# Performance work log

Hardware: AMD Instinct MI355X
Metric: run time of the kernel (lower is better)

## Reference

```python
import jax, jax.numpy as jnp
import numpy as np

B, S, H = 2, 2048, 4096
NQ, NKV, D = 32, 8, 128
THETA = 10000.0


def setup_inputs() -> dict:
    key = jax.random.key(0)
    k0, k1, k2 = jax.random.split(key, 3)
    hidden_states = jax.random.normal(k0, (B, S, H), dtype=jnp.float32)
    w_qkv = jax.random.normal(k1, (H, (NQ + 2 * NKV) * D), dtype=jnp.float32) * 0.02
    w_o = jax.random.normal(k2, (NQ * D, H), dtype=jnp.float32) * 0.02
    positions = jnp.broadcast_to(jnp.arange(S, dtype=jnp.int32)[None, :], (B, S))
    return {"hidden_states": hidden_states, "w_qkv": w_qkv, "w_o": w_o,
            "positions": positions}


def _rope_gptj(x, cos, sin):
    # non-neox (GPT-J interleaved) RoPE; x: [B,S,h,D], cos/sin: [B,S,1,D/2]
    x1 = x[..., 0::2]
    x2 = x[..., 1::2]
    o1 = x1 * cos - x2 * sin
    o2 = x2 * cos + x1 * sin
    return jnp.stack([o1, o2], axis=-1).reshape(x.shape)


def reference(hidden_states, w_qkv, w_o, positions):
    scale = D ** -0.5
    qkv = hidden_states @ w_qkv  # [B,S,(NQ+2NKV)*D]
    q, k, v = jnp.split(qkv, [NQ * D, (NQ + NKV) * D], axis=-1)
    q = q.reshape(B, S, NQ, D)
    k = k.reshape(B, S, NKV, D)
    v = v.reshape(B, S, NKV, D)

    inv_freq = 1.0 / (THETA ** (jnp.arange(0, D, 2, dtype=jnp.float32) / D))
    freqs = positions.astype(jnp.float32)[..., None] * inv_freq  # [B,S,D/2]
    cos = jnp.cos(freqs)[:, :, None, :]
    sin = jnp.sin(freqs)[:, :, None, :]
    q = _rope_gptj(q, cos, sin)
    k = _rope_gptj(k, cos, sin)

    # GQA: expand kv heads to query heads
    rep = NQ // NKV
    k = jnp.repeat(k, rep, axis=2)  # [B,S,NQ,D]
    v = jnp.repeat(v, rep, axis=2)

    scores = jnp.einsum('bqhd,bkhd->bhqk', q, k) * scale
    causal = jnp.tril(jnp.ones((S, S), dtype=bool))
    scores = jnp.where(causal[None, None, :, :], scores, jnp.finfo(scores.dtype).min)
    probs = jax.nn.softmax(scores, axis=-1)
    attn = jnp.einsum('bhqk,bkhd->bqhd', probs, v).reshape(B, S, NQ * D)
    return attn @ w_o  # [B,S,H]
```

## Files before the change

kernel.cpp:

```cpp
#include <hip/hip_runtime.h>
#include <hip/hip_bf16.h>
#include <stdint.h>

#define B_  2
#define S_  2048
#define H_  4096
#define NQ_ 32
#define NKV_ 8
#define D_  128
#define NQKV_ 6144

typedef __bf16 bf16_t;
typedef __bf16 bf16x4 __attribute__((ext_vector_type(4)));
typedef __bf16 bf16x8 __attribute__((ext_vector_type(8)));
typedef float  floatx4 __attribute__((ext_vector_type(4)));

#define GLOBAL_AS __attribute__((address_space(1)))
#define LDS_AS    __attribute__((address_space(3)))

#define QSCALE (0.08838834764831845f * 1.4426950408889634f)

__global__ __launch_bounds__(256) void convert_f32_bf16(
    const float* __restrict__ src, bf16_t* __restrict__ dst, int n4) {
  int i = blockIdx.x * 256 + threadIdx.x;
  if (i < n4) {
    float4 v = ((const float4*)src)[i];
    bf16_t o[4] = {(bf16_t)v.x, (bf16_t)v.y, (bf16_t)v.z, (bf16_t)v.w};
    ((uint64_t*)dst)[i] = *(const uint64_t*)o;
  }
}

__global__ __launch_bounds__(256) void transpose_f32_bf16(
    const float* __restrict__ src, bf16_t* __restrict__ dst, int R, int C) {
  __shared__ bf16_t tile[64][65];
  const int ct = blockIdx.x * 64, rt = blockIdx.y * 64;
  const int t = threadIdx.x;
  const int cl = t & 63;
  for (int i = 0; i < 16; ++i) {
    int rl = i * 4 + (t >> 6);
    tile[rl][cl] = (bf16_t)src[(size_t)(rt + rl) * C + ct + cl];
  }
  __syncthreads();
  const int rl2 = t & 63;
  for (int i = 0; i < 16; ++i) {
    int cl2 = i * 4 + (t >> 6);
    dst[(size_t)(ct + cl2) * R + rt + rl2] = tile[rl2][cl2];
  }
}

template <typename OutT>
__global__ __launch_bounds__(256) void gemm_abt(
    const bf16_t* __restrict__ A, const bf16_t* __restrict__ Bt,
    OutT* __restrict__ C, int M, int N, int K) {
  __shared__ __align__(16) bf16_t lA[128 * 32];
  __shared__ __align__(16) bf16_t lB[128 * 32];
  const int tid = threadIdx.x;
  const int wave = tid >> 6, lane = tid & 63;
  const int lrow = lane & 15, quad = lane >> 4;
  const int row0 = blockIdx.y * 128, col0 = blockIdx.x * 128;
  const int wm = (wave >> 1) * 64, wn = (wave & 1) * 64;
  const int rA = lane >> 2;
  const int kA = (lane & 3) * 8;

  floatx4 acc[4][4] = {};

  for (int kt = 0; kt < K; kt += 32) {
    __syncthreads();
    for (int j = 0; j < 2; ++j) {
      const int c = wave * 2 + j;
      const bf16_t* ga = A  + (size_t)(row0 + c * 16 + rA) * K + kt + kA;
      const bf16_t* gb = Bt + (size_t)(col0 + c * 16 + rA) * K + kt + kA;
      __builtin_amdgcn_global_load_lds((GLOBAL_AS void*)ga,
                                       (LDS_AS void*)(lA + c * 512), 16, 0, 0);
      __builtin_amdgcn_global_load_lds((GLOBAL_AS void*)gb,
                                       (LDS_AS void*)(lB + c * 512), 16, 0, 0);
    }
    __syncthreads();
    bf16x8 af[4], bfr[4];
    for (int i = 0; i < 4; ++i)
      af[i] = *(const bf16x8*)(lA + (wm + i * 16 + lrow) * 32 + quad * 8);
    for (int j = 0; j < 4; ++j)
      bfr[j] = *(const bf16x8*)(lB + (wn + j * 16 + lrow) * 32 + quad * 8);
    for (int i = 0; i < 4; ++i)
      for (int j = 0; j < 4; ++j)
        acc[i][j] = __builtin_amdgcn_mfma_f32_16x16x32_bf16(af[i], bfr[j],
                                                            acc[i][j], 0, 0, 0);
  }

  for (int i = 0; i < 4; ++i)
    for (int j = 0; j < 4; ++j)
      for (int r = 0; r < 4; ++r) {
        int row = row0 + wm + i * 16 + quad * 4 + r;
        int col = col0 + wn + j * 16 + lrow;
        C[(size_t)row * N + col] = (OutT)acc[i][j][r];
      }
}

__global__ __launch_bounds__(256) void rope_qk(
    const bf16_t* __restrict__ qkv, const int* __restrict__ positions,
    bf16_t* __restrict__ Q, bf16_t* __restrict__ K) {
  const int row = blockIdx.x;
  const int b = row >> 11, s = row & (S_ - 1);
  const float pos = (float)positions[row];
  const bf16_t* src = qkv + (size_t)row * NQKV_;
  for (int p = threadIdx.x; p < (NQ_ + NKV_) * 64; p += 256) {
    const int head = p >> 6, i = p & 63;
    const float inv = __powf(10000.0f, -(float)i * (1.0f / 64.0f));
    const float f = pos * inv;
    const float cs = __cosf(f), sn = __sinf(f);
    const float x1 = (float)src[head * 128 + 2 * i];
    const float x2 = (float)src[head * 128 + 2 * i + 1];
    float o1 = x1 * cs - x2 * sn;
    float o2 = x2 * cs + x1 * sn;
    bf16_t* dst;
    if (head < NQ_) {
      o1 *= QSCALE;
      o2 *= QSCALE;
      dst = Q + ((size_t)(b * NQ_ + head) * S_ + s) * D_ + 2 * i;
    } else {
      dst = K + ((size_t)(b * NKV_ + (head - NQ_)) * S_ + s) * D_ + 2 * i;
    }
    dst[0] = (bf16_t)o1;
    dst[1] = (bf16_t)o2;
  }
}

__global__ __launch_bounds__(256) void v_transpose(
    const bf16_t* __restrict__ qkv, bf16_t* __restrict__ Vt) {
  __shared__ bf16_t tile[64][65];
  const int b = blockIdx.z;
  const int kh = blockIdx.y >> 1;
  const int dt = (blockIdx.y & 1) * 64;
  const int st = blockIdx.x * 64;
  const int t = threadIdx.x;
  const int colbase = (NQ_ + NKV_) * D_ + kh * D_ + dt;
  for (int i = 0; i < 16; ++i) {
    int sl = i * 4 + (t >> 6);
    int dl = t & 63;
    tile[sl][dl] = qkv[(size_t)(b * S_ + st + sl) * NQKV_ + colbase + dl];
  }
  __syncthreads();
  for (int i = 0; i < 16; ++i) {
    int dl = i * 4 + (t >> 6);
    int sl = t & 63;
    Vt[((size_t)(b * NKV_ + kh) * D_ + dt + dl) * S_ + st + sl] = tile[sl][dl];
  }
}

__global__ __launch_bounds__(256) void flash_attn(
    const bf16_t* __restrict__ Q, const bf16_t* __restrict__ K,
    const bf16_t* __restrict__ Vt, bf16_t* __restrict__ O) {
  const int qt = (S_ / 64 - 1) - blockIdx.x;
  const int h  = blockIdx.y;
  const int b  = blockIdx.z;
  const int kh = h >> 2;
  const int tid = threadIdx.x, wave = tid >> 6, lane = tid & 63;
  const int lrow = lane & 15, quad = lane >> 4;
  const int q0 = qt * 64;

  __shared__ __align__(16) char lKb[64 * 256];
  __shared__ __align__(16) char lVb[128 * 128];
  __shared__ __align__(16) char lPb[64 * 128];

#define LK(r, c) (lKb + ((r) << 8) + ((c) ^ (((r) & 7) << 4)))
#define LV(r, c) (lVb + ((r) << 7) + ((c) ^ (((r) & 7) << 4)))
#define LP(r, c) (lPb + ((r) << 7) + ((c) ^ (((r) & 7) << 4)))

  const bf16_t* Qbase = Q  + ((size_t)(b * NQ_ + h) * S_) * D_;
  const bf16_t* Kbase = K  + ((size_t)(b * NKV_ + kh) * S_) * D_;
  const bf16_t* Vbase = Vt + ((size_t)(b * NKV_ + kh) * D_) * S_;

  const int qrow = q0 + wave * 16 + lrow;
  bf16x8 qf[4];
  {
    const bf16_t* qp = Qbase + (size_t)qrow * D_ + quad * 8;
    for (int ks = 0; ks < 4; ++ks) qf[ks] = *(const bf16x8*)(qp + ks * 32);
  }

  const int krow = tid >> 4;
  const int kcol = ((((tid & 15) << 4)) ^ ((krow & 7) << 4)) >> 1;
  const int vrow = tid >> 3;
  const int vcol = ((((tid & 7) << 4)) ^ ((vrow & 7) << 4)) >> 1;

  floatx4 acc[8] = {};
  float mrun = -3.0e38f, lrun = 0.0f;

  const int nkt = qt + 1;
  for (int kt = 0; kt < nkt; ++kt) {
    const int k0 = kt * 64;
    __syncthreads();
#pragma unroll
    for (int i = 0; i < 4; ++i) {
      const bf16_t* ga = Kbase + (size_t)(k0 + i * 16 + krow) * D_ + kcol;
      __builtin_amdgcn_global_load_lds((GLOBAL_AS void*)ga,
          (LDS_AS void*)(lKb + i * 4096 + wave * 1024), 16, 0, 0);
    }
#pragma unroll
    for (int i = 0; i < 4; ++i) {
      const bf16_t* ga = Vbase + (size_t)(i * 32 + vrow) * S_ + k0 + vcol;
      __builtin_amdgcn_global_load_lds((GLOBAL_AS void*)ga,
          (LDS_AS void*)(lVb + i * 4096 + wave * 1024), 16, 0, 0);
    }
    __syncthreads();

    floatx4 sacc[4];
#pragma unroll
    for (int t = 0; t < 4; ++t) {
      floatx4 a = {0.f, 0.f, 0.f, 0.f};
#pragma unroll
      for (int ks = 0; ks < 4; ++ks) {
        bf16x8 kf = *(const bf16x8*)LK(t * 16 + lrow, ks * 64 + quad * 16);
        a = __builtin_amdgcn_mfma_f32_16x16x32_bf16(kf, qf[ks], a, 0, 0, 0);
      }
      sacc[t] = a;
    }

    if (kt == qt) {
#pragma unroll
      for (int t = 0; t < 4; ++t)
#pragma unroll
        for (int r = 0; r < 4; ++r) {
          const int kpos = k0 + t * 16 + quad * 4 + r;
          if (kpos > qrow) sacc[t][r] = -3.0e38f;
        }
    }

    float mx = -3.0e38f;
#pragma unroll
    for (int t = 0; t < 4; ++t)
#pragma unroll
      for (int r = 0; r < 4; ++r) mx = fmaxf(mx, sacc[t][r]);
    mx = fmaxf(mx, __shfl_xor(mx, 16));
    mx = fmaxf(mx, __shfl_xor(mx, 32));

    float mcur = mrun;
    if (!__all(mx - mrun <= 8.0f)) {
      const float mnew = fmaxf(mrun, mx);
      const float alpha = exp2f(mrun - mnew);
      lrun *= alpha;
#pragma unroll
      for (int dt = 0; dt < 8; ++dt) acc[dt] *= alpha;
      mrun = mnew;
      mcur = mnew;
    }

    float rs = 0.0f;
#pragma unroll
    for (int t = 0; t < 4; ++t) {
      bf16x4 pk;
#pragma unroll
      for (int r = 0; r < 4; ++r) {
        float p = exp2f(sacc[t][r] - mcur);
        rs += p;
        pk[r] = (bf16_t)p;
      }
      *(bf16x4*)LP(wave * 16 + lrow, t * 32 + quad * 8) = pk;
    }
    rs += __shfl_xor(rs, 16);
    rs += __shfl_xor(rs, 32);
    lrun += rs;

    bf16x8 pf0 = *(const bf16x8*)LP(wave * 16 + lrow, quad * 16);
    bf16x8 pf1 = *(const bf16x8*)LP(wave * 16 + lrow, 64 + quad * 16);
#pragma unroll
    for (int dt = 0; dt < 8; ++dt) {
      bf16x8 v0 = *(const bf16x8*)LV(dt * 16 + lrow, quad * 16);
      bf16x8 v1 = *(const bf16x8*)LV(dt * 16 + lrow, 64 + quad * 16);
      floatx4 a = acc[dt];
      a = __builtin_amdgcn_mfma_f32_16x16x32_bf16(v0, pf0, a, 0, 0, 0);
      a = __builtin_amdgcn_mfma_f32_16x16x32_bf16(v1, pf1, a, 0, 0, 0);
      acc[dt] = a;
    }
  }

  const float inv_l = 1.0f / lrun;
  bf16_t* Obase = O + ((size_t)(b * S_) + qrow) * (NQ_ * D_) + h * D_;
#pragma unroll
  for (int dt = 0; dt < 8; ++dt) {
    bf16x4 ov;
#pragma unroll
    for (int r = 0; r < 4; ++r) ov[r] = (bf16_t)(acc[dt][r] * inv_l);
    *(bf16x4*)(Obase + dt * 16 + quad * 4) = ov;
  }
#undef LK
#undef LV
#undef LP
}

extern "C" void kernel_launch(void* const* d_in, const int* in_sizes, int n_in,
                              void* d_out, int out_size, void* d_ws, size_t ws_size,
                              hipStream_t stream) {
  const float* hs    = (const float*)d_in[0];
  const float* w_qkv = (const float*)d_in[1];
  const float* w_o   = (const float*)d_in[2];
  const int*   pos   = (const int*)d_in[3];
  float* out = (float*)d_out;

  char* ws = (char*)d_ws;
  constexpr size_t OFF_WT  = 0;
  constexpr size_t OFF_QKV = 50331648;
  constexpr size_t OFF_Q   = OFF_QKV + 50331648;
  constexpr size_t OFF_K   = OFF_Q + 33554432;
  constexpr size_t OFF_VT  = OFF_K + 8388608;
  bf16_t* wT    = (bf16_t*)(ws + OFF_WT);
  bf16_t* qkv   = (bf16_t*)(ws + OFF_QKV);
  bf16_t* Qb    = (bf16_t*)(ws + OFF_Q);
  bf16_t* Kb    = (bf16_t*)(ws + OFF_K);
  bf16_t* Vtb   = (bf16_t*)(ws + OFF_VT);
  bf16_t* hsb   = Qb;
  bf16_t* attnO = qkv;

  convert_f32_bf16<<<dim3((B_ * S_ * H_ / 4) / 256), 256, 0, stream>>>(
      hs, hsb, B_ * S_ * H_ / 4);
  transpose_f32_bf16<<<dim3(NQKV_ / 64, H_ / 64), 256, 0, stream>>>(
      w_qkv, wT, H_, NQKV_);
  gemm_abt<bf16_t><<<dim3(NQKV_ / 128, (B_ * S_) / 128), 256, 0, stream>>>(
      hsb, wT, qkv, B_ * S_, NQKV_, H_);
  rope_qk<<<dim3(B_ * S_), 256, 0, stream>>>(qkv, pos, Qb, Kb);
  v_transpose<<<dim3(S_ / 64, NKV_ * 2, B_), 256, 0, stream>>>(qkv, Vtb);
  transpose_f32_bf16<<<dim3(H_ / 64, (NQ_ * D_) / 64), 256, 0, stream>>>(
      w_o, wT, NQ_ * D_, H_);
  flash_attn<<<dim3(S_ / 64, NQ_, B_), 256, 0, stream>>>(Qb, Kb, Vtb, attnO);
  gemm_abt<float><<<dim3(H_ / 128, (B_ * S_) / 128), 256, 0, stream>>>(
      attnO, wT, out, B_ * S_, H_, H_);

  (void)in_sizes; (void)n_in; (void)out_size; (void)ws_size;
}
```

Before: 901.0 us.

## Rewrite GEMM with 256x256 tiles, double-buffered LDS, swizzle and XCD remap

Replaces the 128x128, single-buffered, K=32 GEMM with a 256x256-tile, 512-thread kernel. It uses K=64 steps, double-buffered async global-to-LDS loads with partial vmcnt waits, an XOR-swizzled LDS layout to avoid bank conflicts, and a block-id remap across 8 chiplets. The goal is more data reuse per tile and overlap of loads with MFMA work in both projection GEMMs. In exchange it uses 128KB of LDS per block and more accumulator registers, and the grid shrinks to 384 and 256 blocks, which may leave some compute units idle.

```diff
diff --git a/kernel.cpp b/kernel.cpp
--- a/kernel.cpp
+++ b/kernel.cpp
@@ -49,50 +49,108 @@
 }
 
 template <typename OutT>
-__global__ __launch_bounds__(256) void gemm_abt(
+__global__ __launch_bounds__(512, 2) void gemm_abt256(
     const bf16_t* __restrict__ A, const bf16_t* __restrict__ Bt,
     OutT* __restrict__ C, int M, int N, int K) {
-  __shared__ __align__(16) bf16_t lA[128 * 32];
-  __shared__ __align__(16) bf16_t lB[128 * 32];
+  __shared__ __align__(16) char lds[131072];
+
+  const int nbx = gridDim.x;
+  const int nwg = nbx * gridDim.y;
+  int bid = blockIdx.y * nbx + blockIdx.x;
+  bid = (bid & 7) * (nwg >> 3) + (bid >> 3);
+  const int bx = bid % nbx, by = bid / nbx;
+
   const int tid = threadIdx.x;
   const int wave = tid >> 6, lane = tid & 63;
   const int lrow = lane & 15, quad = lane >> 4;
-  const int row0 = blockIdx.y * 128, col0 = blockIdx.x * 128;
-  const int wm = (wave >> 1) * 64, wn = (wave & 1) * 64;
-  const int rA = lane >> 2;
-  const int kA = (lane & 3) * 8;
-
-  floatx4 acc[4][4] = {};
-
-  for (int kt = 0; kt < K; kt += 32) {
-    __syncthreads();
-    for (int j = 0; j < 2; ++j) {
-      const int c = wave * 2 + j;
-      const bf16_t* ga = A  + (size_t)(row0 + c * 16 + rA) * K + kt + kA;
-      const bf16_t* gb = Bt + (size_t)(col0 + c * 16 + rA) * K + kt + kA;
-      __builtin_amdgcn_global_load_lds((GLOBAL_AS void*)ga,
-                                       (LDS_AS void*)(lA + c * 512), 16, 0, 0);
-      __builtin_amdgcn_global_load_lds((GLOBAL_AS void*)gb,
-                                       (LDS_AS void*)(lB + c * 512), 16, 0, 0);
-    }
-    __syncthreads();
-    bf16x8 af[4], bfr[4];
-    for (int i = 0; i < 4; ++i)
-      af[i] = *(const bf16x8*)(lA + (wm + i * 16 + lrow) * 32 + quad * 8);
-    for (int j = 0; j < 4; ++j)
-      bfr[j] = *(const bf16x8*)(lB + (wn + j * 16 + lrow) * 32 + quad * 8);
-    for (int i = 0; i < 4; ++i)
-      for (int j = 0; j < 4; ++j)
-        acc[i][j] = __builtin_amdgcn_mfma_f32_16x16x32_bf16(af[i], bfr[j],
-                                                            acc[i][j], 0, 0, 0);
-  }
-
-  for (int i = 0; i < 4; ++i)
-    for (int j = 0; j < 4; ++j)
+  const int wm = (wave >> 2) * 128;
+  const int wn = (wave & 3) * 64;
+  const int row0 = by * 256, col0 = bx * 256;
+
+  const int lr = lane >> 3;
+  const int lc = ((((lane & 7) << 4) ^ (lr << 4)) >> 1);
+
+  auto stage = [&](int buf, int kt) {
+    char* aB = lds + buf * 65536;
+    char* bB = aB + 32768;
+#pragma unroll
+    for (int h = 0; h < 2; ++h)
+#pragma unroll
+      for (int i = 0; i < 2; ++i) {
+        const bf16_t* ga =
+            A + (size_t)(row0 + h * 128 + i * 64 + wave * 8 + lr) * K + kt + lc;
+        __builtin_amdgcn_global_load_lds(
+            (GLOBAL_AS void*)ga,
+            (LDS_AS void*)(aB + h * 16384 + i * 8192 + wave * 1024), 16, 0, 0);
+      }
+#pragma unroll
+    for (int h = 0; h < 2; ++h)
+#pragma unroll
+      for (int i = 0; i < 2; ++i) {
+        const bf16_t* gb =
+            Bt + (size_t)(col0 + h * 128 + i * 64 + wave * 8 + lr) * K + kt + lc;
+        __builtin_amdgcn_global_load_lds(
+            (GLOBAL_AS void*)gb,
+            (LDS_AS void*)(bB + h * 16384 + i * 8192 + wave * 1024), 16, 0, 0);
+      }
+  };
+
+  floatx4 acc[8][4] = {};
+  const int nt = K >> 6;
+  const int sw = (lrow & 7) << 4;
+
+  stage(0, 0);
+  int cur = 0;
+  for (int t = 0; t < nt; ++t) {
+    if (t + 1 < nt) stage(cur ^ 1, (t + 1) * 64);
+    __builtin_amdgcn_sched_barrier(0);
+    if (t + 1 < nt)
+      asm volatile("s_waitcnt vmcnt(8)" ::: "memory");
+    else
+      asm volatile("s_waitcnt vmcnt(0)" ::: "memory");
+    __builtin_amdgcn_s_barrier();
+    __builtin_amdgcn_sched_barrier(0);
+
+    const char* aB = lds + cur * 65536;
+    const char* bB = aB + 32768;
+    __builtin_amdgcn_s_setprio(1);
+#pragma unroll
+    for (int kk = 0; kk < 2; ++kk) {
+      bf16x8 af[8], bfr[4];
+#pragma unroll
+      for (int fm = 0; fm < 8; ++fm) {
+        const int r = wm + fm * 16 + lrow;
+        af[fm] = *(const bf16x8*)(aB + r * 128 + ((kk * 64 + quad * 16) ^ sw));
+      }
+#pragma unroll
+      for (int fn = 0; fn < 4; ++fn) {
+        const int r = wn + fn * 16 + lrow;
+        bfr[fn] = *(const bf16x8*)(bB + r * 128 + ((kk * 64 + quad * 16) ^ sw));
+      }
+#pragma unroll
+      for (int fm = 0; fm < 8; ++fm)
+#pragma unroll
+        for (int fn = 0; fn < 4; ++fn)
+          acc[fm][fn] = __builtin_amdgcn_mfma_f32_16x16x32_bf16(
+              af[fm], bfr[fn], acc[fm][fn], 0, 0, 0);
+    }
+    __builtin_amdgcn_s_setprio(0);
+
+    asm volatile("s_waitcnt lgkmcnt(0)" ::: "memory");
+    __builtin_amdgcn_s_barrier();
+    __builtin_amdgcn_sched_barrier(0);
+    cur ^= 1;
+  }
+
+#pragma unroll
+  for (int fm = 0; fm < 8; ++fm)
+#pragma unroll
+    for (int fn = 0; fn < 4; ++fn)
+#pragma unroll
       for (int r = 0; r < 4; ++r) {
-        int row = row0 + wm + i * 16 + quad * 4 + r;
-        int col = col0 + wn + j * 16 + lrow;
-        C[(size_t)row * N + col] = (OutT)acc[i][j][r];
+        int row = row0 + wm + fm * 16 + quad * 4 + r;
+        int col = col0 + wn + fn * 16 + lrow;
+        C[(size_t)row * N + col] = (OutT)acc[fm][fn][r];
       }
 }
 
@@ -314,14 +372,14 @@
       hs, hsb, B_ * S_ * H_ / 4);
   transpose_f32_bf16<<<dim3(NQKV_ / 64, H_ / 64), 256, 0, stream>>>(
       w_qkv, wT, H_, NQKV_);
-  gemm_abt<bf16_t><<<dim3(NQKV_ / 128, (B_ * S_) / 128), 256, 0, stream>>>(
+  gemm_abt256<bf16_t><<<dim3(NQKV_ / 256, (B_ * S_) / 256), 512, 0, stream>>>(
       hsb, wT, qkv, B_ * S_, NQKV_, H_);
   rope_qk<<<dim3(B_ * S_), 256, 0, stream>>>(qkv, pos, Qb, Kb);
   v_transpose<<<dim3(S_ / 64, NKV_ * 2, B_), 256, 0, stream>>>(qkv, Vtb);
   transpose_f32_bf16<<<dim3(H_ / 64, (NQ_ * D_) / 64), 256, 0, stream>>>(
       w_o, wT, NQ_ * D_, H_);
   flash_attn<<<dim3(S_ / 64, NQ_, B_), 256, 0, stream>>>(Qb, Kb, Vtb, attnO);
-  gemm_abt<float><<<dim3(H_ / 128, (B_ * S_) / 128), 256, 0, stream>>>(
+  gemm_abt256<float><<<dim3(H_ / 256, (B_ * S_) / 256), 512, 0, stream>>>(
       attnO, wT, out, B_ * S_, H_, H_);
 
   (void)in_sizes; (void)n_in; (void)out_size; (void)ws_size;
```

Measured after the change: 827.1 us. -8.2%, faster.
